# Kernel tuning notes

Measured on AMD Instinct MI355X. Metric: run time of the kernel, lower is better.

## Reference

```python
import jax, jax.numpy as jnp
import numpy as np

BUCKET_SIZE = 64
B, H, N, D = 4, 16, 4096, 64

def _perm(key, shape):
    # per-(b,h) random permutation of positions, like LSH bucket sort order
    return jnp.argsort(jax.random.uniform(key, shape), axis=-1).astype(jnp.int64)

def setup_inputs() -> dict:
    key = jax.random.key(0)
    k1, k2, k3, k4, k5 = jax.random.split(key, 5)
    return {
        "query": jax.random.normal(k1, (B, H, N, D), dtype=jnp.float32),
        "key": jax.random.normal(k2, (B, H, N, D), dtype=jnp.float32),
        "weight": jax.random.normal(k3, (B, H, N, D), dtype=jnp.float32),
        "K_sort_idx": _perm(k4, (B, H, N)),
        "Q_sort_idx": _perm(k5, (B, H, N)),
    }

def _select(matrix, indices):
    # matrix: [B,H,N,D], indices: [B,H,N] -> gather along axis 2
    return jnp.take_along_axis(matrix, indices[..., None], axis=2)

def reference(query, key, weight, K_sort_idx, Q_sort_idx):
    bucket = BUCKET_SIZE
    b, h, nq, d = query.shape
    nk, dv = key.shape[2], weight.shape[3]
    num_blocks = nk // bucket
    q_bucket = nq // num_blocks

    q_sorted = _select(query, Q_sort_idx)      # [B,H,Nq,D]
    k_sorted = _select(key, K_sort_idx)        # [B,H,Nk,D]
    w_sorted = _select(weight, K_sort_idx)     # [B,H,Nk,Dv]

    qb = q_sorted.reshape(-1, q_bucket, d)     # [B*H*nb, qb, D]
    kb = k_sorted.reshape(-1, bucket, d)       # [B*H*nb, bk, D]
    wb = w_sorted.reshape(-1, bucket, dv)      # [B*H*nb, bk, Dv]

    A = jnp.exp(jnp.einsum('bnd,bmd->bnm', qb, kb))  # [B*H*nb, qb, bk]
    res = jnp.einsum('bnm,bmv->bnv', A, wb)          # [B*H*nb, qb, Dv]
    res = res.reshape(b, h, nq, dv)

    Q_inv = jnp.argsort(Q_sort_idx, axis=2)    # inverse permutation
    return _select(res, Q_inv)
```

## Files before the change

kernel.cpp:

```cpp
#include <hip/hip_runtime.h>


constexpr int Nc      = 4096;
constexpr int Dc      = 64;
constexpr int BUCKETc = 64;
constexpr int NBc     = Nc / BUCKETc;
constexpr int LD      = 68;

__global__ __launch_bounds__(256, 3)
void lsh_bucket_attn(const float* __restrict__ query,
                     const float* __restrict__ key,
                     const float* __restrict__ weight,
                     const int*   __restrict__ K_sort_idx,
                     const int*   __restrict__ Q_sort_idx,
                     float*       __restrict__ out)
{
    __shared__ __align__(16) float QsT[Dc][LD];
    __shared__ __align__(16) float KsT[Dc][LD];
    __shared__ __align__(16) float Wsh[BUCKETc][LD];
    __shared__ int qpos[BUCKETc];

    const int wg  = blockIdx.x;
    const int bh  = wg >> 6;
    const int blk = wg & (NBc - 1);
    const int t   = threadIdx.x;
    const int tc  = t & 15;
    const int tr  = t >> 4;

    const size_t rowbase = (size_t)bh * Nc;
    const int    idxbase = bh * Nc + blk * BUCKETc;

    #pragma unroll
    for (int p = 0; p < 4; ++p) {
        const int r  = (p << 4) + tr;
        const int qi = Q_sort_idx[idxbase + r];
        const int ki = K_sort_idx[idxbase + r];
        if (tc == 0) qpos[r] = qi;
        const int c4 = tc << 2;
        const float4 q4 = *(const float4*)(query  + (rowbase + qi) * Dc + c4);
        const float4 k4 = *(const float4*)(key    + (rowbase + ki) * Dc + c4);
        const float4 w4 = *(const float4*)(weight + (rowbase + ki) * Dc + c4);
        QsT[c4 + 0][r] = q4.x; QsT[c4 + 1][r] = q4.y;
        QsT[c4 + 2][r] = q4.z; QsT[c4 + 3][r] = q4.w;
        KsT[c4 + 0][r] = k4.x; KsT[c4 + 1][r] = k4.y;
        KsT[c4 + 2][r] = k4.z; KsT[c4 + 3][r] = k4.w;
        *(float4*)&Wsh[r][c4] = w4;
    }
    __syncthreads();

    const int tx = tc;
    const int ty = tr;

    float s[4][4] = {};
    #pragma unroll 8
    for (int k = 0; k < Dc; ++k) {
        const float4 a4 = *(const float4*)&QsT[k][ty << 2];
        const float4 b4 = *(const float4*)&KsT[k][tx << 2];
        const float a[4] = {a4.x, a4.y, a4.z, a4.w};
        const float b[4] = {b4.x, b4.y, b4.z, b4.w};
        #pragma unroll
        for (int i = 0; i < 4; ++i)
            #pragma unroll
            for (int j = 0; j < 4; ++j)
                s[i][j] += a[i] * b[j];
    }
    __syncthreads();

    #pragma unroll
    for (int i = 0; i < 4; ++i)
        #pragma unroll
        for (int j = 0; j < 4; ++j)
            QsT[(tx << 2) + j][(ty << 2) + i] = expf(s[i][j]);
    __syncthreads();

    float r[4][4] = {};
    #pragma unroll 8
    for (int k = 0; k < BUCKETc; ++k) {
        const float4 a4 = *(const float4*)&QsT[k][ty << 2];
        const float4 b4 = *(const float4*)&Wsh[k][tx << 2];
        const float a[4] = {a4.x, a4.y, a4.z, a4.w};
        const float b[4] = {b4.x, b4.y, b4.z, b4.w};
        #pragma unroll
        for (int i = 0; i < 4; ++i)
            #pragma unroll
            for (int j = 0; j < 4; ++j)
                r[i][j] += a[i] * b[j];
    }

    #pragma unroll
    for (int i = 0; i < 4; ++i) {
        const int n   = (ty << 2) + i;
        const int pos = qpos[n];
        const float4 o = {r[i][0], r[i][1], r[i][2], r[i][3]};
        *(float4*)(out + (rowbase + pos) * Dc + (tx << 2)) = o;
    }
}

extern "C" void kernel_launch(void* const* d_in, const int* in_sizes, int n_in,
                              void* d_out, int out_size, void* d_ws, size_t ws_size,
                              hipStream_t stream) {
    const float* query  = (const float*)d_in[0];
    const float* key    = (const float*)d_in[1];
    const float* weight = (const float*)d_in[2];
    const int*   kidx   = (const int*)d_in[3];
    const int*   qidx   = (const int*)d_in[4];
    float*       out    = (float*)d_out;

    const int BH = in_sizes[3] / Nc;
    const int grid = BH * NBc;
    lsh_bucket_attn<<<grid, 256, 0, stream>>>(query, key, weight, kidx, qidx, out);
}
```

Measured before the change: 231.0 us.

## Rewrite bucket attention with bf16 split-precision MFMA, one wave per bucket

```diff
diff --git a/kernel.cpp b/kernel.cpp
--- a/kernel.cpp
+++ b/kernel.cpp
@@ -1,98 +1,195 @@
 #include <hip/hip_runtime.h>
 
 
-constexpr int Nc      = 4096;
-constexpr int Dc      = 64;
-constexpr int BUCKETc = 64;
-constexpr int NBc     = Nc / BUCKETc;
-constexpr int LD      = 68;
-
-__global__ __launch_bounds__(256, 3)
-void lsh_bucket_attn(const float* __restrict__ query,
-                     const float* __restrict__ key,
-                     const float* __restrict__ weight,
-                     const int*   __restrict__ K_sort_idx,
-                     const int*   __restrict__ Q_sort_idx,
-                     float*       __restrict__ out)
+typedef __attribute__((ext_vector_type(8)))  short bf16x8;
+typedef __attribute__((ext_vector_type(16))) float f32x16;
+
+constexpr int Nc  = 4096;
+constexpr int Dc  = 64;
+constexpr int LDA = 66;
+constexpr int WPB = 3;
+
+union FragU { uint u[4]; bf16x8 v; };
+
+__device__ __forceinline__ uint bfh(float x) {
+    uint u = __float_as_uint(x);
+    return (u + 0x7fffu + ((u >> 16) & 1u)) >> 16;
+}
+__device__ __forceinline__ float bf2f(uint h) { return __uint_as_float(h << 16); }
+
+__device__ __forceinline__ void split2(float x0, float x1, uint& hp, uint& lp) {
+    uint h0 = bfh(x0), h1 = bfh(x1);
+    float r0 = x0 - bf2f(h0);
+    float r1 = x1 - bf2f(h1);
+    uint l0 = bfh(r0), l1 = bfh(r1);
+    hp = h0 | (h1 << 16);
+    lp = l0 | (l1 << 16);
+}
+
+#define MFMA32(A, B, C) __builtin_amdgcn_mfma_f32_32x32x16_bf16((A), (B), (C), 0, 0, 0)
+
+__global__ __launch_bounds__(WPB * 64)
+void lsh_mfma_kernel(const float* __restrict__ Qg, const float* __restrict__ Kg,
+                     const float* __restrict__ Wg, const int* __restrict__ Kidx,
+                     const int* __restrict__ Qidx, float* __restrict__ Og,
+                     int nbuck)
 {
-    __shared__ __align__(16) float QsT[Dc][LD];
-    __shared__ __align__(16) float KsT[Dc][LD];
-    __shared__ __align__(16) float Wsh[BUCKETc][LD];
-    __shared__ int qpos[BUCKETc];
-
-    const int wg  = blockIdx.x;
-    const int bh  = wg >> 6;
-    const int blk = wg & (NBc - 1);
-    const int t   = threadIdx.x;
-    const int tc  = t & 15;
-    const int tr  = t >> 4;
-
-    const size_t rowbase = (size_t)bh * Nc;
-    const int    idxbase = bh * Nc + blk * BUCKETc;
-
-    #pragma unroll
-    for (int p = 0; p < 4; ++p) {
-        const int r  = (p << 4) + tr;
-        const int qi = Q_sort_idx[idxbase + r];
-        const int ki = K_sort_idx[idxbase + r];
-        if (tc == 0) qpos[r] = qi;
-        const int c4 = tc << 2;
-        const float4 q4 = *(const float4*)(query  + (rowbase + qi) * Dc + c4);
-        const float4 k4 = *(const float4*)(key    + (rowbase + ki) * Dc + c4);
-        const float4 w4 = *(const float4*)(weight + (rowbase + ki) * Dc + c4);
-        QsT[c4 + 0][r] = q4.x; QsT[c4 + 1][r] = q4.y;
-        QsT[c4 + 2][r] = q4.z; QsT[c4 + 3][r] = q4.w;
-        KsT[c4 + 0][r] = k4.x; KsT[c4 + 1][r] = k4.y;
-        KsT[c4 + 2][r] = k4.z; KsT[c4 + 3][r] = k4.w;
-        *(float4*)&Wsh[r][c4] = w4;
-    }
-    __syncthreads();
-
-    const int tx = tc;
-    const int ty = tr;
-
-    float s[4][4] = {};
-    #pragma unroll 8
-    for (int k = 0; k < Dc; ++k) {
-        const float4 a4 = *(const float4*)&QsT[k][ty << 2];
-        const float4 b4 = *(const float4*)&KsT[k][tx << 2];
-        const float a[4] = {a4.x, a4.y, a4.z, a4.w};
-        const float b[4] = {b4.x, b4.y, b4.z, b4.w};
-        #pragma unroll
-        for (int i = 0; i < 4; ++i)
+    __shared__ uint Apk[WPB][64][LDA];
+    __shared__ int  kposL[WPB][64];
+    __shared__ int  qposL[WPB][64];
+
+    const int wv   = threadIdx.x >> 6;
+    const int lane = threadIdx.x & 63;
+    const int bucket = blockIdx.x * WPB + wv;
+    if (bucket >= nbuck) return;
+
+    const int bh  = bucket >> 6;
+    const int blk = bucket & 63;
+    const size_t base = (size_t)bh * (size_t)(Nc * Dc);
+    const int ib = bh * Nc + blk * 64;
+
+    const int c32 = lane & 31;
+    const int h   = lane >> 5;
+
+    kposL[wv][lane] = Kidx[ib + lane];
+    qposL[wv][lane] = Qidx[ib + lane];
+
+    FragU qh[2][4], ql[2][4];
+    #pragma unroll
+    for (int ti = 0; ti < 2; ++ti) {
+        const int qrow = qposL[wv][32 * ti + c32];
+        const float* p = Qg + base + (size_t)qrow * Dc + 8 * h;
+        #pragma unroll
+        for (int ks = 0; ks < 4; ++ks) {
+            const float4 a = *(const float4*)(p + 16 * ks);
+            const float4 b = *(const float4*)(p + 16 * ks + 4);
+            split2(a.x, a.y, qh[ti][ks].u[0], ql[ti][ks].u[0]);
+            split2(a.z, a.w, qh[ti][ks].u[1], ql[ti][ks].u[1]);
+            split2(b.x, b.y, qh[ti][ks].u[2], ql[ti][ks].u[2]);
+            split2(b.z, b.w, qh[ti][ks].u[3], ql[ti][ks].u[3]);
+        }
+    }
+
+    f32x16 S00 = (f32x16)0.0f, S01 = (f32x16)0.0f;
+    f32x16 S10 = (f32x16)0.0f, S11 = (f32x16)0.0f;
+
+    #pragma unroll
+    for (int tj = 0; tj < 2; ++tj) {
+        FragU kh[4], kl[4];
+        const int krow = kposL[wv][32 * tj + c32];
+        const float* p = Kg + base + (size_t)krow * Dc + 8 * h;
+        #pragma unroll
+        for (int ks = 0; ks < 4; ++ks) {
+            const float4 a = *(const float4*)(p + 16 * ks);
+            const float4 b = *(const float4*)(p + 16 * ks + 4);
+            split2(a.x, a.y, kh[ks].u[0], kl[ks].u[0]);
+            split2(a.z, a.w, kh[ks].u[1], kl[ks].u[1]);
+            split2(b.x, b.y, kh[ks].u[2], kl[ks].u[2]);
+            split2(b.z, b.w, kh[ks].u[3], kl[ks].u[3]);
+        }
+        #pragma unroll
+        for (int ks = 0; ks < 4; ++ks) {
+            if (tj == 0) {
+                S00 = MFMA32(qh[0][ks].v, kh[ks].v, S00);
+                S00 = MFMA32(qh[0][ks].v, kl[ks].v, S00);
+                S00 = MFMA32(ql[0][ks].v, kh[ks].v, S00);
+                S10 = MFMA32(qh[1][ks].v, kh[ks].v, S10);
+                S10 = MFMA32(qh[1][ks].v, kl[ks].v, S10);
+                S10 = MFMA32(ql[1][ks].v, kh[ks].v, S10);
+            } else {
+                S01 = MFMA32(qh[0][ks].v, kh[ks].v, S01);
+                S01 = MFMA32(qh[0][ks].v, kl[ks].v, S01);
+                S01 = MFMA32(ql[0][ks].v, kh[ks].v, S01);
+                S11 = MFMA32(qh[1][ks].v, kh[ks].v, S11);
+                S11 = MFMA32(qh[1][ks].v, kl[ks].v, S11);
+                S11 = MFMA32(ql[1][ks].v, kh[ks].v, S11);
+            }
+        }
+    }
+
+    #pragma unroll
+    for (int r = 0; r < 16; ++r) {
+        const int rb = 4 * h + (r & 3) + 8 * (r >> 2);
+        const float a00 = __expf(S00[r]);
+        const float a01 = __expf(S01[r]);
+        const float a10 = __expf(S10[r]);
+        const float a11 = __expf(S11[r]);
+        const uint h00 = bfh(a00), l00 = bfh(a00 - bf2f(h00));
+        const uint h01 = bfh(a01), l01 = bfh(a01 - bf2f(h01));
+        const uint h10 = bfh(a10), l10 = bfh(a10 - bf2f(h10));
+        const uint h11 = bfh(a11), l11 = bfh(a11 - bf2f(h11));
+        Apk[wv][rb][c32]           = h00 | (l00 << 16);
+        Apk[wv][rb][32 + c32]      = h01 | (l01 << 16);
+        Apk[wv][32 + rb][c32]      = h10 | (l10 << 16);
+        Apk[wv][32 + rb][32 + c32] = h11 | (l11 << 16);
+    }
+
+    FragU wh[2][4], wl[2][4];
+    #pragma unroll
+    for (int tj = 0; tj < 2; ++tj) {
+        #pragma unroll
+        for (int ks = 0; ks < 4; ++ks) {
             #pragma unroll
-            for (int j = 0; j < 4; ++j)
-                s[i][j] += a[i] * b[j];
-    }
-    __syncthreads();
-
-    #pragma unroll
-    for (int i = 0; i < 4; ++i)
-        #pragma unroll
-        for (int j = 0; j < 4; ++j)
-            QsT[(tx << 2) + j][(ty << 2) + i] = expf(s[i][j]);
-    __syncthreads();
-
-    float r[4][4] = {};
-    #pragma unroll 8
-    for (int k = 0; k < BUCKETc; ++k) {
-        const float4 a4 = *(const float4*)&QsT[k][ty << 2];
-        const float4 b4 = *(const float4*)&Wsh[k][tx << 2];
-        const float a[4] = {a4.x, a4.y, a4.z, a4.w};
-        const float b[4] = {b4.x, b4.y, b4.z, b4.w};
-        #pragma unroll
-        for (int i = 0; i < 4; ++i)
-            #pragma unroll
-            for (int j = 0; j < 4; ++j)
-                r[i][j] += a[i] * b[j];
-    }
-
-    #pragma unroll
-    for (int i = 0; i < 4; ++i) {
-        const int n   = (ty << 2) + i;
-        const int pos = qpos[n];
-        const float4 o = {r[i][0], r[i][1], r[i][2], r[i][3]};
-        *(float4*)(out + (rowbase + pos) * Dc + (tx << 2)) = o;
+            for (int j = 0; j < 4; ++j) {
+                const int m0 = 16 * ks + 8 * h + 2 * j;
+                const int r0 = kposL[wv][m0];
+                const int r1 = kposL[wv][m0 + 1];
+                const float x0 = Wg[base + (size_t)r0 * Dc + 32 * tj + c32];
+                const float x1 = Wg[base + (size_t)r1 * Dc + 32 * tj + c32];
+                split2(x0, x1, wh[tj][ks].u[j], wl[tj][ks].u[j]);
+            }
+        }
+    }
+
+    f32x16 R00 = (f32x16)0.0f, R01 = (f32x16)0.0f;
+    f32x16 R10 = (f32x16)0.0f, R11 = (f32x16)0.0f;
+
+    #pragma unroll
+    for (int ti = 0; ti < 2; ++ti) {
+        #pragma unroll
+        for (int ks = 0; ks < 4; ++ks) {
+            const uint* pr = &Apk[wv][32 * ti + c32][16 * ks + 8 * h];
+            const uint2 u0 = *(const uint2*)(pr + 0);
+            const uint2 u1 = *(const uint2*)(pr + 2);
+            const uint2 u2 = *(const uint2*)(pr + 4);
+            const uint2 u3 = *(const uint2*)(pr + 6);
+            FragU ah, al;
+            ah.u[0] = (u0.x & 0xffffu) | (u0.y << 16);
+            al.u[0] = (u0.x >> 16)     | (u0.y & 0xffff0000u);
+            ah.u[1] = (u1.x & 0xffffu) | (u1.y << 16);
+            al.u[1] = (u1.x >> 16)     | (u1.y & 0xffff0000u);
+            ah.u[2] = (u2.x & 0xffffu) | (u2.y << 16);
+            al.u[2] = (u2.x >> 16)     | (u2.y & 0xffff0000u);
+            ah.u[3] = (u3.x & 0xffffu) | (u3.y << 16);
+            al.u[3] = (u3.x >> 16)     | (u3.y & 0xffff0000u);
+            if (ti == 0) {
+                R00 = MFMA32(ah.v, wh[0][ks].v, R00);
+                R00 = MFMA32(ah.v, wl[0][ks].v, R00);
+                R00 = MFMA32(al.v, wh[0][ks].v, R00);
+                R01 = MFMA32(ah.v, wh[1][ks].v, R01);
+                R01 = MFMA32(ah.v, wl[1][ks].v, R01);
+                R01 = MFMA32(al.v, wh[1][ks].v, R01);
+            } else {
+                R10 = MFMA32(ah.v, wh[0][ks].v, R10);
+                R10 = MFMA32(ah.v, wl[0][ks].v, R10);
+                R10 = MFMA32(al.v, wh[0][ks].v, R10);
+                R11 = MFMA32(ah.v, wh[1][ks].v, R11);
+                R11 = MFMA32(ah.v, wl[1][ks].v, R11);
+                R11 = MFMA32(al.v, wh[1][ks].v, R11);
+            }
+        }
+    }
+
+    #pragma unroll
+    for (int ti = 0; ti < 2; ++ti) {
+        #pragma unroll
+        for (int r = 0; r < 16; ++r) {
+            const int row  = 32 * ti + 4 * h + (r & 3) + 8 * (r >> 2);
+            const int orow = qposL[wv][row];
+            float* po = Og + base + (size_t)orow * Dc;
+            po[c32]      = (ti == 0) ? R00[r] : R10[r];
+            po[32 + c32] = (ti == 0) ? R01[r] : R11[r];
+        }
     }
 }
 
@@ -106,7 +203,8 @@
     const int*   qidx   = (const int*)d_in[4];
     float*       out    = (float*)d_out;
 
-    const int BH = in_sizes[3] / Nc;
-    const int grid = BH * NBc;
-    lsh_bucket_attn<<<grid, 256, 0, stream>>>(query, key, weight, kidx, qidx, out);
-}
+    const int BH    = in_sizes[3] / Nc;
+    const int nbuck = BH * (Nc / 64);
+    const int blocks = (nbuck + WPB - 1) / WPB;
+    lsh_mfma_kernel<<<blocks, WPB * 64, 0, stream>>>(query, key, weight, kidx, qidx, out, nbuck);
+}
```

Measured after the change: 221.8 us. 4.0% less time.

## Rewrite bucket attention with split-bf16 MFMA, one wave per bucket

Applied to the files above, without the earlier changes.

```diff
diff --git a/kernel.cpp b/kernel.cpp
--- a/kernel.cpp
+++ b/kernel.cpp
@@ -1,98 +1,143 @@
 #include <hip/hip_runtime.h>
 
 
-constexpr int Nc      = 4096;
-constexpr int Dc      = 64;
-constexpr int BUCKETc = 64;
-constexpr int NBc     = Nc / BUCKETc;
-constexpr int LD      = 68;
+typedef __attribute__((ext_vector_type(8)))  short bf16x8;
+typedef __attribute__((ext_vector_type(16))) float f32x16;
 
-__global__ __launch_bounds__(256, 3)
-void lsh_bucket_attn(const float* __restrict__ query,
-                     const float* __restrict__ key,
-                     const float* __restrict__ weight,
-                     const int*   __restrict__ K_sort_idx,
-                     const int*   __restrict__ Q_sort_idx,
-                     float*       __restrict__ out)
+constexpr int Nc  = 4096;
+constexpr int Dc  = 64;
+constexpr int WPB = 4;
+
+union FragU { uint u[4]; bf16x8 v; };
+
+__device__ __forceinline__ uint cvtpk(float a, float b) {
+    uint r;
+    asm("v_cvt_pk_bf16_f32 %0, %1, %2" : "=v"(r) : "v"(a), "v"(b));
+    return r;
+}
+__device__ __forceinline__ void plswap(uint& d, uint& s) {
+    asm("v_permlane32_swap_b32 %0, %1" : "+&v"(d), "+&v"(s));
+}
+__device__ __forceinline__ void split2(float x0, float x1, uint& hp, uint& lp) {
+    hp = cvtpk(x0, x1);
+    const float h0 = __uint_as_float(hp << 16);
+    const float h1 = __uint_as_float(hp & 0xffff0000u);
+    lp = cvtpk(x0 - h0, x1 - h1);
+}
+__device__ __forceinline__ void load8split(const float* p, FragU& hi, FragU& lo) {
+    const float4 a = *(const float4*)p;
+    const float4 b = *(const float4*)(p + 4);
+    split2(a.x, a.y, hi.u[0], lo.u[0]);
+    split2(a.z, a.w, hi.u[1], lo.u[1]);
+    split2(b.x, b.y, hi.u[2], lo.u[2]);
+    split2(b.z, b.w, hi.u[3], lo.u[3]);
+}
+#define MFMA32(A, B, C) __builtin_amdgcn_mfma_f32_32x32x16_bf16((A), (B), (C), 0, 0, 0)
+
+__global__ __launch_bounds__(WPB * 64, 3)
+void lsh_mfma3(const float* __restrict__ Qg, const float* __restrict__ Kg,
+               const float* __restrict__ Wg, const int* __restrict__ Kidx,
+               const int* __restrict__ Qidx, float* __restrict__ Og, int nbuck)
 {
-    __shared__ __align__(16) float QsT[Dc][LD];
-    __shared__ __align__(16) float KsT[Dc][LD];
-    __shared__ __align__(16) float Wsh[BUCKETc][LD];
-    __shared__ int qpos[BUCKETc];
+    __shared__ int kposL[WPB][64];
+    __shared__ int qposL[WPB][64];
 
-    const int wg  = blockIdx.x;
-    const int bh  = wg >> 6;
-    const int blk = wg & (NBc - 1);
-    const int t   = threadIdx.x;
-    const int tc  = t & 15;
-    const int tr  = t >> 4;
+    const int wv   = threadIdx.x >> 6;
+    const int lane = threadIdx.x & 63;
+    const int bucket = blockIdx.x * WPB + wv;
+    if (bucket >= nbuck) return;
 
-    const size_t rowbase = (size_t)bh * Nc;
-    const int    idxbase = bh * Nc + blk * BUCKETc;
+    const int bh  = bucket >> 6;
+    const int blk = bucket & 63;
+    const size_t base = (size_t)bh * (size_t)(Nc * Dc);
+    const int ib  = bh * Nc + blk * 64;
+    const int c32 = lane & 31;
+    const int h   = lane >> 5;
+    const int dh  = 8 * h;
 
+    const int ki = Kidx[ib + lane];
+    const int qi = Qidx[ib + lane];
+    kposL[wv][lane] = ki;
+    qposL[wv][lane] = qi;
+
+    uint ka = (uint)ki, kb = (uint)ki; plswap(ka, kb);
+    uint qa = (uint)qi, qb = (uint)qi; plswap(qa, qb);
+
+    const float* kp0 = Kg + base + (size_t)ka * Dc + dh;
+    const float* kp1 = Kg + base + (size_t)kb * Dc + dh;
+    const float* qp0 = Qg + base + (size_t)qa * Dc + dh;
+    const float* qp1 = Qg + base + (size_t)qb * Dc + dh;
+
+    f32x16 T00 = (f32x16)0.f, T01 = (f32x16)0.f, T10 = (f32x16)0.f, T11 = (f32x16)0.f;
     #pragma unroll
-    for (int p = 0; p < 4; ++p) {
-        const int r  = (p << 4) + tr;
-        const int qi = Q_sort_idx[idxbase + r];
-        const int ki = K_sort_idx[idxbase + r];
-        if (tc == 0) qpos[r] = qi;
-        const int c4 = tc << 2;
-        const float4 q4 = *(const float4*)(query  + (rowbase + qi) * Dc + c4);
-        const float4 k4 = *(const float4*)(key    + (rowbase + ki) * Dc + c4);
-        const float4 w4 = *(const float4*)(weight + (rowbase + ki) * Dc + c4);
-        QsT[c4 + 0][r] = q4.x; QsT[c4 + 1][r] = q4.y;
-        QsT[c4 + 2][r] = q4.z; QsT[c4 + 3][r] = q4.w;
-        KsT[c4 + 0][r] = k4.x; KsT[c4 + 1][r] = k4.y;
-        KsT[c4 + 2][r] = k4.z; KsT[c4 + 3][r] = k4.w;
-        *(float4*)&Wsh[r][c4] = w4;
-    }
-    __syncthreads();
-
-    const int tx = tc;
-    const int ty = tr;
-
-    float s[4][4] = {};
-    #pragma unroll 8
-    for (int k = 0; k < Dc; ++k) {
-        const float4 a4 = *(const float4*)&QsT[k][ty << 2];
-        const float4 b4 = *(const float4*)&KsT[k][tx << 2];
-        const float a[4] = {a4.x, a4.y, a4.z, a4.w};
-        const float b[4] = {b4.x, b4.y, b4.z, b4.w};
-        #pragma unroll
-        for (int i = 0; i < 4; ++i)
-            #pragma unroll
-            for (int j = 0; j < 4; ++j)
-                s[i][j] += a[i] * b[j];
-    }
-    __syncthreads();
-
-    #pragma unroll
-    for (int i = 0; i < 4; ++i)
-        #pragma unroll
-        for (int j = 0; j < 4; ++j)
-            QsT[(tx << 2) + j][(ty << 2) + i] = expf(s[i][j]);
-    __syncthreads();
-
-    float r[4][4] = {};
-    #pragma unroll 8
-    for (int k = 0; k < BUCKETc; ++k) {
-        const float4 a4 = *(const float4*)&QsT[k][ty << 2];
-        const float4 b4 = *(const float4*)&Wsh[k][tx << 2];
-        const float a[4] = {a4.x, a4.y, a4.z, a4.w};
-        const float b[4] = {b4.x, b4.y, b4.z, b4.w};
-        #pragma unroll
-        for (int i = 0; i < 4; ++i)
-            #pragma unroll
-            for (int j = 0; j < 4; ++j)
-                r[i][j] += a[i] * b[j];
+    for (int ks = 0; ks < 4; ++ks) {
+        FragU kh0, kl0, kh1, kl1, qh0, ql0, qh1, ql1;
+        load8split(kp0 + 16 * ks, kh0, kl0);
+        load8split(kp1 + 16 * ks, kh1, kl1);
+        load8split(qp0 + 16 * ks, qh0, ql0);
+        load8split(qp1 + 16 * ks, qh1, ql1);
+        T00 = MFMA32(kh0.v, qh0.v, T00); T00 = MFMA32(kh0.v, ql0.v, T00); T00 = MFMA32(kl0.v, qh0.v, T00);
+        T01 = MFMA32(kh0.v, qh1.v, T01); T01 = MFMA32(kh0.v, ql1.v, T01); T01 = MFMA32(kl0.v, qh1.v, T01);
+        T10 = MFMA32(kh1.v, qh0.v, T10); T10 = MFMA32(kh1.v, ql0.v, T10); T10 = MFMA32(kl1.v, qh0.v, T10);
+        T11 = MFMA32(kh1.v, qh1.v, T11); T11 = MFMA32(kh1.v, ql1.v, T11); T11 = MFMA32(kl1.v, qh1.v, T11);
     }
 
+    FragU ah[2][4], al[2][4];
     #pragma unroll
-    for (int i = 0; i < 4; ++i) {
-        const int n   = (ty << 2) + i;
-        const int pos = qpos[n];
-        const float4 o = {r[i][0], r[i][1], r[i][2], r[i][3]};
-        *(float4*)(out + (rowbase + pos) * Dc + (tx << 2)) = o;
+    for (int ks = 0; ks < 4; ++ks) {
+        const int rb = 8 * (ks & 1);
+        #pragma unroll
+        for (int nt = 0; nt < 2; ++nt) {
+            const f32x16& T = (ks < 2) ? (nt ? T01 : T00) : (nt ? T11 : T10);
+            const float a0 = __expf(T[rb + 0]), a1 = __expf(T[rb + 1]);
+            const float a2 = __expf(T[rb + 2]), a3 = __expf(T[rb + 3]);
+            const float a4 = __expf(T[rb + 4]), a5 = __expf(T[rb + 5]);
+            const float a6 = __expf(T[rb + 6]), a7 = __expf(T[rb + 7]);
+            FragU H, L;
+            split2(a0, a1, H.u[0], L.u[0]);
+            split2(a2, a3, H.u[1], L.u[1]);
+            split2(a4, a5, H.u[2], L.u[2]);
+            split2(a6, a7, H.u[3], L.u[3]);
+            plswap(H.u[0], H.u[2]); plswap(H.u[1], H.u[3]);
+            plswap(L.u[0], L.u[2]); plswap(L.u[1], L.u[3]);
+            ah[nt][ks] = H; al[nt][ks] = L;
+        }
+    }
+
+    f32x16 R00 = (f32x16)0.f, R01 = (f32x16)0.f, R10 = (f32x16)0.f, R11 = (f32x16)0.f;
+    const float* Wb = Wg + base;
+    #pragma unroll
+    for (int ks = 0; ks < 4; ++ks) {
+        FragU wh0, wl0, wh1, wl1;
+        #pragma unroll
+        for (int j = 0; j < 4; ++j) {
+            const int m0 = 16 * ks + dh + 2 * j;
+            const int r0 = kposL[wv][m0];
+            const int r1 = kposL[wv][m0 + 1];
+            const float* w0 = Wb + (size_t)r0 * Dc + c32;
+            const float* w1 = Wb + (size_t)r1 * Dc + c32;
+            split2(w0[0],  w1[0],  wh0.u[j], wl0.u[j]);
+            split2(w0[32], w1[32], wh1.u[j], wl1.u[j]);
+        }
+        R00 = MFMA32(ah[0][ks].v, wh0.v, R00); R00 = MFMA32(ah[0][ks].v, wl0.v, R00); R00 = MFMA32(al[0][ks].v, wh0.v, R00);
+        R01 = MFMA32(ah[0][ks].v, wh1.v, R01); R01 = MFMA32(ah[0][ks].v, wl1.v, R01); R01 = MFMA32(al[0][ks].v, wh1.v, R01);
+        R10 = MFMA32(ah[1][ks].v, wh0.v, R10); R10 = MFMA32(ah[1][ks].v, wl0.v, R10); R10 = MFMA32(al[1][ks].v, wh0.v, R10);
+        R11 = MFMA32(ah[1][ks].v, wh1.v, R11); R11 = MFMA32(ah[1][ks].v, wl1.v, R11); R11 = MFMA32(al[1][ks].v, wh1.v, R11);
+    }
+
+    float* Ob = Og + base;
+    #pragma unroll
+    for (int nt = 0; nt < 2; ++nt) {
+        const f32x16& Ra = nt ? R10 : R00;
+        const f32x16& Rb = nt ? R11 : R01;
+        #pragma unroll
+        for (int r = 0; r < 16; ++r) {
+            const int n    = 32 * nt + 4 * h + (r & 3) + 8 * (r >> 2);
+            const int orow = qposL[wv][n];
+            float* po = Ob + (size_t)orow * Dc;
+            po[c32]      = Ra[r];
+            po[32 + c32] = Rb[r];
+        }
     }
 }
 
@@ -106,7 +151,8 @@
     const int*   qidx   = (const int*)d_in[4];
     float*       out    = (float*)d_out;
 
-    const int BH = in_sizes[3] / Nc;
-    const int grid = BH * NBc;
-    lsh_bucket_attn<<<grid, 256, 0, stream>>>(query, key, weight, kidx, qidx, out);
+    const int BH     = in_sizes[3] / Nc;
+    const int nbuck  = BH * (Nc / 64);
+    const int blocks = (nbuck + WPB - 1) / WPB;
+    lsh_mfma3<<<blocks, WPB * 64, 0, stream>>>(query, key, weight, kidx, qidx, out, nbuck);
 }
```

Measured after the change: 227.4 us. Within noise of the previous version (-1.6%).
